# Performance work log

Hardware: AMD Instinct MI355X
Metric: run time of the kernel (lower is better)

Reference implementation:

```python
import jax, jax.numpy as jnp
import numpy as np

DMODEL = 1024
N_EXPERTS = 8
EXPERT_SIZE = 4096
TOPK = 2
B, S = 2, 2048


def setup_inputs() -> dict:
    key = jax.random.key(0)
    ks = jax.random.split(key, 6)
    std = EXPERT_SIZE ** (-0.5)  # init_expert_weights: normal(0, expert_size**-0.5 * weight_scale)
    x = jax.random.normal(ks[0], (B, S, DMODEL), dtype=jnp.float32)
    gate_w = 0.02 * jax.random.normal(ks[1], (N_EXPERTS, DMODEL), dtype=jnp.float32)
    w1 = std * jax.random.normal(ks[2], (N_EXPERTS, EXPERT_SIZE, DMODEL), dtype=jnp.float32)
    b1 = jnp.zeros((N_EXPERTS, EXPERT_SIZE), dtype=jnp.float32)
    w2 = std * jax.random.normal(ks[3], (N_EXPERTS, DMODEL, EXPERT_SIZE), dtype=jnp.float32)
    b2 = jnp.zeros((N_EXPERTS, DMODEL), dtype=jnp.float32)
    return {"x": x, "gate_w": gate_w, "w1": w1, "b1": b1, "w2": w2, "b2": b2}


def reference(x, gate_w, w1, b1, w2, b2):
    # Router: gate linear (no bias) -> softmax -> top-k expert selection
    logits = jnp.einsum('bsd,ed->bse', x, gate_w)          # [B,S,E]
    probs = jax.nn.softmax(logits, axis=-1)                # gate_softmax
    top_w, top_i = jax.lax.top_k(probs, TOPK)              # [B,S,K]
    # Scatter top-k weights back to a dense [B,S,E] routing matrix
    route = jnp.sum(jax.nn.one_hot(top_i, N_EXPERTS, dtype=probs.dtype)
                    * top_w[..., None], axis=-2)           # [B,S,E]
    # Per-expert 2-layer MLP (Linear -> ReLU -> Linear), combined by route weights
    out = jnp.zeros_like(x)
    for e in range(N_EXPERTS):
        h = jax.nn.relu(jnp.einsum('bsd,hd->bsh', x, w1[e]) + b1[e])  # [B,S,H]
        y = jnp.einsum('bsh,dh->bsd', h, w2[e]) + b2[e]               # [B,S,D]
        out = out + route[..., e, None] * y
    return out
```

## Files before the change

kernel.cpp:

```cpp
#include <hip/hip_runtime.h>
#include <hip/hip_bf16.h>
#include <stdint.h>

#define DMODEL 1024
#define NEXP   8
#define HSZ    4096
#define NTOK   4096

typedef __attribute__((ext_vector_type(8))) short bf16x8;
typedef __attribute__((ext_vector_type(4))) float f32x4;

__device__ __forceinline__ unsigned short f2bf(float f) {
  union { float f; unsigned u; } v; v.f = f;
  return (unsigned short)((v.u + 0x8000u) >> 16);
}

__device__ __forceinline__ void gl2lds16(const void* g, void* lds) {
  __builtin_amdgcn_global_load_lds(
      (const __attribute__((address_space(1))) unsigned*)g,
      (__attribute__((address_space(3))) unsigned*)lds, 16, 0, 0);
}

__global__ __launch_bounds__(256) void cvt_all_kernel(
    const float* __restrict__ x, const float* __restrict__ w1,
    const float* __restrict__ w2, unsigned short* __restrict__ xb,
    unsigned short* __restrict__ w1b, unsigned short* __restrict__ w2b) {
  const size_t n0 = (size_t)NTOK * DMODEL / 4;
  const size_t n1 = (size_t)NEXP * HSZ * DMODEL / 4;
  size_t i = (size_t)blockIdx.x * 256 + threadIdx.x;
  const float* src; unsigned short* dst; size_t j;
  if (i < n0)            { src = x;  dst = xb;  j = i; }
  else if (i < n0 + n1)  { src = w1; dst = w1b; j = i - n0; }
  else                   { src = w2; dst = w2b; j = i - n0 - n1; }
  float4 v = ((const float4*)src)[j];
  ((ushort4*)dst)[j] = make_ushort4(f2bf(v.x), f2bf(v.y), f2bf(v.z), f2bf(v.w));
}

__global__ __launch_bounds__(256) void router_kernel(
    const float* __restrict__ x, const float* __restrict__ gw,
    int* __restrict__ cnt, int* __restrict__ tokl, float* __restrict__ twgt,
    int* __restrict__ sidx) {
  int wave = threadIdx.x >> 6;
  int lane = threadIdx.x & 63;
  int t = blockIdx.x * 4 + wave;
  const float* xr = x + (size_t)t * DMODEL;
  float acc[NEXP];
#pragma unroll
  for (int e = 0; e < NEXP; ++e) acc[e] = 0.f;
  for (int d = lane; d < DMODEL; d += 64) {
    float xv = xr[d];
#pragma unroll
    for (int e = 0; e < NEXP; ++e) acc[e] = fmaf(xv, gw[e * DMODEL + d], acc[e]);
  }
#pragma unroll
  for (int e = 0; e < NEXP; ++e) {
#pragma unroll
    for (int o = 32; o > 0; o >>= 1) acc[e] += __shfl_down(acc[e], o);
  }
  if (lane == 0) {
    float m = acc[0];
#pragma unroll
    for (int e = 1; e < NEXP; ++e) m = fmaxf(m, acc[e]);
    float p[NEXP]; float s = 0.f;
#pragma unroll
    for (int e = 0; e < NEXP; ++e) { p[e] = __expf(acc[e] - m); s += p[e]; }
    float inv = 1.f / s;
    int i0 = 0; float b0 = p[0];
#pragma unroll
    for (int e = 1; e < NEXP; ++e) if (p[e] > b0) { b0 = p[e]; i0 = e; }
    int i1 = (i0 == 0) ? 1 : 0; float b1v = p[i1];
#pragma unroll
    for (int e = 0; e < NEXP; ++e) if (e != i0 && p[e] > b1v) { b1v = p[e]; i1 = e; }
    int p0 = atomicAdd(&cnt[i0], 1);
    tokl[i0 * NTOK + p0] = t; twgt[i0 * NTOK + p0] = b0 * inv;
    int p1 = atomicAdd(&cnt[i1], 1);
    tokl[i1 * NTOK + p1] = t; twgt[i1 * NTOK + p1] = b1v * inv;
    sidx[2 * t]     = (i0 << 16) | p0;
    sidx[2 * t + 1] = (i1 << 16) | p1;
  }
}

__global__ __launch_bounds__(256) void gemm1_bf_kernel(
    const unsigned short* __restrict__ Xbf, const unsigned short* __restrict__ W1bf,
    const float* __restrict__ b1, const int* __restrict__ cnt,
    const int* __restrict__ tokl, unsigned short* __restrict__ Hbuf) {
  const int e = blockIdx.z;
  const int ne = cnt[e];
  const int m0 = blockIdx.y * 128;
  if (m0 >= ne) return;
  const int n0 = blockIdx.x * 128;
  int toff = 0;
  for (int i = 0; i < NEXP; ++i) toff += (i < e) ? cnt[i] : 0;

  __shared__ __align__(16) unsigned short As[2][128 * 32];
  __shared__ __align__(16) unsigned short Bs[2][128 * 32];

  const int tid = threadIdx.x;
  const int lane = tid & 63;
  const int wave = tid >> 6;
  const int wm = (wave >> 1) * 64;
  const int wn = (wave & 1) * 64;

  const int srow = wave * 16 + (lane >> 2);
  const int scol = (((lane & 3) ^ ((lane >> 3) & 3)) << 3);
  const int* tlist = tokl + e * NTOK;
  const unsigned short* gA[2]; const unsigned short* gB[2];
  int lofs[2];
#pragma unroll
  for (int c = 0; c < 2; ++c) {
    int r = c * 64 + srow;
    int gr = m0 + r;
    int tk = tlist[(gr < ne) ? gr : 0];
    gA[c] = Xbf + (size_t)tk * DMODEL + scol;
    gB[c] = W1bf + (size_t)e * HSZ * DMODEL + (size_t)(n0 + r) * DMODEL + scol;
    lofs[c] = (c * 64 + wave * 16) * 32;
  }

  f32x4 acc[4][4];
#pragma unroll
  for (int i = 0; i < 4; ++i)
#pragma unroll
    for (int j = 0; j < 4; ++j) acc[i][j] = (f32x4){0.f, 0.f, 0.f, 0.f};

  const int fr = lane & 15;
  const int cb = lane >> 4;

#pragma unroll
  for (int c = 0; c < 2; ++c) {
    gl2lds16(gA[c], &As[0][lofs[c]]);
    gl2lds16(gB[c], &Bs[0][lofs[c]]);
  }
  __syncthreads();

  int cur = 0;
  for (int k0 = 0; k0 < DMODEL; k0 += 32) {
    const int nxt = k0 + 32;
    if (nxt < DMODEL) {
#pragma unroll
      for (int c = 0; c < 2; ++c) {
        gl2lds16(gA[c] + nxt, &As[cur ^ 1][lofs[c]]);
        gl2lds16(gB[c] + nxt, &Bs[cur ^ 1][lofs[c]]);
      }
    }
    bf16x8 af[4], bfg[4];
#pragma unroll
    for (int i = 0; i < 4; ++i) {
      int ar = wm + i * 16 + fr;
      af[i]  = *(const bf16x8*)&As[cur][ar * 32 + ((cb ^ ((ar >> 1) & 3)) << 3)];
      int br = wn + i * 16 + fr;
      bfg[i] = *(const bf16x8*)&Bs[cur][br * 32 + ((cb ^ ((br >> 1) & 3)) << 3)];
    }
#pragma unroll
    for (int i = 0; i < 4; ++i)
#pragma unroll
      for (int j = 0; j < 4; ++j)
        acc[i][j] = __builtin_amdgcn_mfma_f32_16x16x32_bf16(bfg[j], af[i], acc[i][j], 0, 0, 0);
    __syncthreads();
    cur ^= 1;
  }

  const int hq = (lane >> 4) * 4;
#pragma unroll
  for (int i = 0; i < 4; ++i) {
    int trow = m0 + wm + i * 16 + fr;
    if (trow >= ne) continue;
    size_t hrow = (size_t)(toff + trow) * HSZ;
#pragma unroll
    for (int j = 0; j < 4; ++j) {
      int hcol = n0 + wn + j * 16 + hq;
      const float* bp = b1 + e * HSZ + hcol;
      unsigned short u[4];
#pragma unroll
      for (int r = 0; r < 4; ++r)
        u[r] = f2bf(fmaxf(acc[i][j][r] + bp[r], 0.f));
      *(ushort4*)&Hbuf[hrow + hcol] = make_ushort4(u[0], u[1], u[2], u[3]);
    }
  }
}

__global__ __launch_bounds__(256) void gemm2_bf_kernel(
    const unsigned short* __restrict__ Hbuf, const unsigned short* __restrict__ W2bf,
    const float* __restrict__ b2, const int* __restrict__ cnt,
    const float* __restrict__ twgt, float* __restrict__ Ybuf) {
  const int e = blockIdx.z;
  const int ne = cnt[e];
  const int m0 = blockIdx.y * 128;
  if (m0 >= ne) return;
  const int n0 = blockIdx.x * 128;
  int toff = 0;
  for (int i = 0; i < NEXP; ++i) toff += (i < e) ? cnt[i] : 0;

  __shared__ __align__(16) unsigned short As[2][128 * 64];
  __shared__ __align__(16) unsigned short Bs[2][128 * 64];

  const int tid = threadIdx.x;
  const int lane = tid & 63;
  const int wave = tid >> 6;
  const int wm = (wave >> 1) * 64;
  const int wn = (wave & 1) * 64;

  const int srow = (wave << 5) + (lane >> 3);
  const int scb  = (((lane & 7) ^ (lane >> 3)) << 3);
  const unsigned short* gA[4]; const unsigned short* gB[4];
  int lofs[4];
#pragma unroll
  for (int c = 0; c < 4; ++c) {
    int r = srow + c * 8;
    int gr = m0 + r;
    int rc = (gr < ne) ? gr : 0;
    gA[c] = Hbuf + (size_t)(toff + rc) * HSZ + scb;
    gB[c] = W2bf + (size_t)e * DMODEL * HSZ + (size_t)(n0 + r) * HSZ + scb;
    lofs[c] = ((wave << 5) + c * 8) * 64;
  }

  f32x4 acc[4][4];
#pragma unroll
  for (int i = 0; i < 4; ++i)
#pragma unroll
    for (int j = 0; j < 4; ++j) acc[i][j] = (f32x4){0.f, 0.f, 0.f, 0.f};

  const int fr = lane & 15;
  const int cb0 = lane >> 4;

#pragma unroll
  for (int c = 0; c < 4; ++c) {
    gl2lds16(gA[c], &As[0][lofs[c]]);
    gl2lds16(gB[c], &Bs[0][lofs[c]]);
  }
  __syncthreads();

  int cur = 0;
  for (int k0 = 0; k0 < HSZ; k0 += 64) {
    const int nxt = k0 + 64;
    if (nxt < HSZ) {
#pragma unroll
      for (int c = 0; c < 4; ++c) {
        gl2lds16(gA[c] + nxt, &As[cur ^ 1][lofs[c]]);
        gl2lds16(gB[c] + nxt, &Bs[cur ^ 1][lofs[c]]);
      }
    }
    bf16x8 af[2][4], bfg[2][4];
#pragma unroll
    for (int h = 0; h < 2; ++h) {
      int cb = cb0 + h * 4;
#pragma unroll
      for (int i = 0; i < 4; ++i) {
        int ar = wm + i * 16 + fr;
        af[h][i]  = *(const bf16x8*)&As[cur][ar * 64 + ((cb ^ (ar & 7)) << 3)];
        int br = wn + i * 16 + fr;
        bfg[h][i] = *(const bf16x8*)&Bs[cur][br * 64 + ((cb ^ (br & 7)) << 3)];
      }
    }
#pragma unroll
    for (int h = 0; h < 2; ++h)
#pragma unroll
      for (int i = 0; i < 4; ++i)
#pragma unroll
        for (int j = 0; j < 4; ++j)
          acc[i][j] = __builtin_amdgcn_mfma_f32_16x16x32_bf16(bfg[h][j], af[h][i],
                                                              acc[i][j], 0, 0, 0);
    __syncthreads();
    cur ^= 1;
  }

  const float* wlist = twgt + e * NTOK;
  const int dq = (lane >> 4) * 4;
#pragma unroll
  for (int i = 0; i < 4; ++i) {
    int trow = m0 + wm + i * 16 + fr;
    if (trow >= ne) continue;
    float wgt = wlist[trow];
    float* yrow = Ybuf + (size_t)(toff + trow) * DMODEL;
#pragma unroll
    for (int j = 0; j < 4; ++j) {
      int d0 = n0 + wn + j * 16 + dq;
      const float* b2p = b2 + e * DMODEL + d0;
      float4 v = make_float4(wgt * (acc[i][j][0] + b2p[0]),
                             wgt * (acc[i][j][1] + b2p[1]),
                             wgt * (acc[i][j][2] + b2p[2]),
                             wgt * (acc[i][j][3] + b2p[3]));
      *(float4*)(yrow + d0) = v;
    }
  }
}

__global__ __launch_bounds__(256) void combine_kernel(
    const float* __restrict__ Ybuf, const int* __restrict__ cnt,
    const int* __restrict__ sidx, float* __restrict__ out) {
  int t = blockIdx.x;
  int offv[NEXP];
  int s = 0;
#pragma unroll
  for (int e = 0; e < NEXP; ++e) { offv[e] = s; s += cnt[e]; }
  int s0 = sidx[2 * t], s1 = sidx[2 * t + 1];
  size_t r0 = (size_t)(offv[s0 >> 16] + (s0 & 0xffff)) * DMODEL;
  size_t r1 = (size_t)(offv[s1 >> 16] + (s1 & 0xffff)) * DMODEL;
  int c = threadIdx.x * 4;
  float4 a = *(const float4*)(Ybuf + r0 + c);
  float4 b = *(const float4*)(Ybuf + r1 + c);
  *(float4*)(out + (size_t)t * DMODEL + c) =
      make_float4(a.x + b.x, a.y + b.y, a.z + b.z, a.w + b.w);
}

extern "C" void kernel_launch(void* const* d_in, const int* in_sizes, int n_in,
                              void* d_out, int out_size, void* d_ws, size_t ws_size,
                              hipStream_t stream) {
  const float* x  = (const float*)d_in[0];
  const float* gw = (const float*)d_in[1];
  const float* w1 = (const float*)d_in[2];
  const float* b1 = (const float*)d_in[3];
  const float* w2 = (const float*)d_in[4];
  const float* b2 = (const float*)d_in[5];
  float* out = (float*)d_out;

  char* ws = (char*)d_ws;
  int* cnt    = (int*)ws;
  int* tokl   = (int*)(ws + 128);
  float* twgt = (float*)(ws + 128 + NEXP * NTOK * 4);
  int* sidx   = (int*)(ws + 128 + 2 * NEXP * NTOK * 4);

  constexpr size_t OFF_XBF  = 327680;
  constexpr size_t OFF_W1BF = OFF_XBF  + (size_t)NTOK * DMODEL * 2;
  constexpr size_t OFF_W2BF = OFF_W1BF + (size_t)NEXP * HSZ * DMODEL * 2;
  constexpr size_t OFF_HBUF = OFF_W2BF + (size_t)NEXP * DMODEL * HSZ * 2;
  unsigned short* Xbf  = (unsigned short*)(ws + OFF_XBF);
  unsigned short* W1bf = (unsigned short*)(ws + OFF_W1BF);
  unsigned short* W2bf = (unsigned short*)(ws + OFF_W2BF);
  unsigned short* Hbuf = (unsigned short*)(ws + OFF_HBUF);
  float* Ybuf = (float*)(ws + OFF_W1BF);

  hipMemsetAsync(cnt, 0, 32, stream);
  router_kernel<<<NTOK / 4, 256, 0, stream>>>(x, gw, cnt, tokl, twgt, sidx);
  const size_t ncvt = (size_t)NTOK * DMODEL / 4 + 2 * (size_t)NEXP * HSZ * DMODEL / 4;
  cvt_all_kernel<<<(unsigned)((ncvt + 255) / 256), 256, 0, stream>>>(
      x, w1, w2, Xbf, W1bf, W2bf);
  gemm1_bf_kernel<<<dim3(HSZ / 128, NTOK / 128, NEXP), 256, 0, stream>>>(
      Xbf, W1bf, b1, cnt, tokl, Hbuf);
  gemm2_bf_kernel<<<dim3(DMODEL / 128, NTOK / 128, NEXP), 256, 0, stream>>>(
      Hbuf, W2bf, b2, cnt, twgt, Ybuf);
  combine_kernel<<<NTOK, 256, 0, stream>>>(Ybuf, cnt, sidx, out);
}
```

Measured before the change: 673.8 us.

## Split-K the second expert GEMM and batch router atomics per block

```diff
diff --git a/kernel.cpp b/kernel.cpp
--- a/kernel.cpp
+++ b/kernel.cpp
@@ -6,6 +6,7 @@
 #define NEXP   8
 #define HSZ    4096
 #define NTOK   4096
+#define KSPLIT 2
 
 typedef __attribute__((ext_vector_type(8))) short bf16x8;
 typedef __attribute__((ext_vector_type(4))) float f32x4;
@@ -40,43 +41,64 @@
     const float* __restrict__ x, const float* __restrict__ gw,
     int* __restrict__ cnt, int* __restrict__ tokl, float* __restrict__ twgt,
     int* __restrict__ sidx) {
-  int wave = threadIdx.x >> 6;
-  int lane = threadIdx.x & 63;
-  int t = blockIdx.x * 4 + wave;
-  const float* xr = x + (size_t)t * DMODEL;
-  float acc[NEXP];
-#pragma unroll
-  for (int e = 0; e < NEXP; ++e) acc[e] = 0.f;
-  for (int d = lane; d < DMODEL; d += 64) {
-    float xv = xr[d];
-#pragma unroll
-    for (int e = 0; e < NEXP; ++e) acc[e] = fmaf(xv, gw[e * DMODEL + d], acc[e]);
-  }
-#pragma unroll
-  for (int e = 0; e < NEXP; ++e) {
-#pragma unroll
-    for (int o = 32; o > 0; o >>= 1) acc[e] += __shfl_down(acc[e], o);
-  }
-  if (lane == 0) {
-    float m = acc[0];
-#pragma unroll
-    for (int e = 1; e < NEXP; ++e) m = fmaxf(m, acc[e]);
-    float p[NEXP]; float s = 0.f;
-#pragma unroll
-    for (int e = 0; e < NEXP; ++e) { p[e] = __expf(acc[e] - m); s += p[e]; }
-    float inv = 1.f / s;
-    int i0 = 0; float b0 = p[0];
-#pragma unroll
-    for (int e = 1; e < NEXP; ++e) if (p[e] > b0) { b0 = p[e]; i0 = e; }
-    int i1 = (i0 == 0) ? 1 : 0; float b1v = p[i1];
-#pragma unroll
-    for (int e = 0; e < NEXP; ++e) if (e != i0 && p[e] > b1v) { b1v = p[e]; i1 = e; }
-    int p0 = atomicAdd(&cnt[i0], 1);
-    tokl[i0 * NTOK + p0] = t; twgt[i0 * NTOK + p0] = b0 * inv;
-    int p1 = atomicAdd(&cnt[i1], 1);
-    tokl[i1 * NTOK + p1] = t; twgt[i1 * NTOK + p1] = b1v * inv;
-    sidx[2 * t]     = (i0 << 16) | p0;
-    sidx[2 * t + 1] = (i1 << 16) | p1;
+  __shared__ int lcnt[NEXP];
+  __shared__ int lbase[NEXP];
+  __shared__ int rE[64];
+  __shared__ int rS[64];
+  __shared__ float rW[64];
+  const int tid = threadIdx.x;
+  const int wave = tid >> 6;
+  const int lane = tid & 63;
+  if (tid < NEXP) lcnt[tid] = 0;
+  __syncthreads();
+
+  for (int i = 0; i < 8; ++i) {
+    int lt = wave * 8 + i;
+    int t = blockIdx.x * 32 + lt;
+    const float* xr = x + (size_t)t * DMODEL;
+    float acc[NEXP];
+#pragma unroll
+    for (int e = 0; e < NEXP; ++e) acc[e] = 0.f;
+    for (int d = lane; d < DMODEL; d += 64) {
+      float xv = xr[d];
+#pragma unroll
+      for (int e = 0; e < NEXP; ++e) acc[e] = fmaf(xv, gw[e * DMODEL + d], acc[e]);
+    }
+#pragma unroll
+    for (int e = 0; e < NEXP; ++e) {
+#pragma unroll
+      for (int o = 32; o > 0; o >>= 1) acc[e] += __shfl_down(acc[e], o);
+    }
+    if (lane == 0) {
+      float m = acc[0];
+#pragma unroll
+      for (int e = 1; e < NEXP; ++e) m = fmaxf(m, acc[e]);
+      float p[NEXP]; float s = 0.f;
+#pragma unroll
+      for (int e = 0; e < NEXP; ++e) { p[e] = __expf(acc[e] - m); s += p[e]; }
+      float inv = 1.f / s;
+      int i0 = 0; float b0 = p[0];
+#pragma unroll
+      for (int e = 1; e < NEXP; ++e) if (p[e] > b0) { b0 = p[e]; i0 = e; }
+      int i1 = (i0 == 0) ? 1 : 0; float b1v = p[i1];
+#pragma unroll
+      for (int e = 0; e < NEXP; ++e) if (e != i0 && p[e] > b1v) { b1v = p[e]; i1 = e; }
+      int s0l = atomicAdd(&lcnt[i0], 1);
+      rE[lt * 2] = i0; rS[lt * 2] = s0l; rW[lt * 2] = b0 * inv;
+      int s1l = atomicAdd(&lcnt[i1], 1);
+      rE[lt * 2 + 1] = i1; rS[lt * 2 + 1] = s1l; rW[lt * 2 + 1] = b1v * inv;
+    }
+  }
+  __syncthreads();
+  if (tid < NEXP) lbase[tid] = atomicAdd(&cnt[tid], lcnt[tid]);
+  __syncthreads();
+  if (tid < 64) {
+    int e = rE[tid];
+    int p = lbase[e] + rS[tid];
+    int t = blockIdx.x * 32 + (tid >> 1);
+    tokl[e * NTOK + p] = t;
+    twgt[e * NTOK + p] = rW[tid];
+    sidx[2 * t + (tid & 1)] = (e << 16) | p;
   }
 }
 
@@ -180,18 +202,20 @@
 
 __global__ __launch_bounds__(256) void gemm2_bf_kernel(
     const unsigned short* __restrict__ Hbuf, const unsigned short* __restrict__ W2bf,
-    const float* __restrict__ b2, const int* __restrict__ cnt,
-    const float* __restrict__ twgt, float* __restrict__ Ybuf) {
-  const int e = blockIdx.z;
+    const int* __restrict__ cnt, const float* __restrict__ twgt,
+    float* __restrict__ Ybuf) {
+  const int e = blockIdx.z & 7;
+  const int ks = blockIdx.z >> 3;
   const int ne = cnt[e];
   const int m0 = blockIdx.y * 128;
   if (m0 >= ne) return;
   const int n0 = blockIdx.x * 128;
+  const int kbase = ks * (HSZ / KSPLIT);
   int toff = 0;
   for (int i = 0; i < NEXP; ++i) toff += (i < e) ? cnt[i] : 0;
 
-  __shared__ __align__(16) unsigned short As[2][128 * 64];
-  __shared__ __align__(16) unsigned short Bs[2][128 * 64];
+  __shared__ __align__(16) unsigned short As[2][128 * 32];
+  __shared__ __align__(16) unsigned short Bs[2][128 * 32];
 
   const int tid = threadIdx.x;
   const int lane = tid & 63;
@@ -199,18 +223,18 @@
   const int wm = (wave >> 1) * 64;
   const int wn = (wave & 1) * 64;
 
-  const int srow = (wave << 5) + (lane >> 3);
-  const int scb  = (((lane & 7) ^ (lane >> 3)) << 3);
-  const unsigned short* gA[4]; const unsigned short* gB[4];
-  int lofs[4];
-#pragma unroll
-  for (int c = 0; c < 4; ++c) {
-    int r = srow + c * 8;
+  const int srow = wave * 16 + (lane >> 2);
+  const int scol = (((lane & 3) ^ ((lane >> 3) & 3)) << 3);
+  const unsigned short* gA[2]; const unsigned short* gB[2];
+  int lofs[2];
+#pragma unroll
+  for (int c = 0; c < 2; ++c) {
+    int r = c * 64 + srow;
     int gr = m0 + r;
     int rc = (gr < ne) ? gr : 0;
-    gA[c] = Hbuf + (size_t)(toff + rc) * HSZ + scb;
-    gB[c] = W2bf + (size_t)e * DMODEL * HSZ + (size_t)(n0 + r) * HSZ + scb;
-    lofs[c] = ((wave << 5) + c * 8) * 64;
+    gA[c] = Hbuf + (size_t)(toff + rc) * HSZ + kbase + scol;
+    gB[c] = W2bf + (size_t)e * DMODEL * HSZ + (size_t)(n0 + r) * HSZ + kbase + scol;
+    lofs[c] = (c * 64 + wave * 16) * 32;
   }
 
   f32x4 acc[4][4];
@@ -220,86 +244,90 @@
     for (int j = 0; j < 4; ++j) acc[i][j] = (f32x4){0.f, 0.f, 0.f, 0.f};
 
   const int fr = lane & 15;
-  const int cb0 = lane >> 4;
-
-#pragma unroll
-  for (int c = 0; c < 4; ++c) {
+  const int cb = lane >> 4;
+
+#pragma unroll
+  for (int c = 0; c < 2; ++c) {
     gl2lds16(gA[c], &As[0][lofs[c]]);
     gl2lds16(gB[c], &Bs[0][lofs[c]]);
   }
   __syncthreads();
 
   int cur = 0;
-  for (int k0 = 0; k0 < HSZ; k0 += 64) {
-    const int nxt = k0 + 64;
-    if (nxt < HSZ) {
-#pragma unroll
-      for (int c = 0; c < 4; ++c) {
+  for (int k0 = 0; k0 < HSZ / KSPLIT; k0 += 32) {
+    const int nxt = k0 + 32;
+    if (nxt < HSZ / KSPLIT) {
+#pragma unroll
+      for (int c = 0; c < 2; ++c) {
         gl2lds16(gA[c] + nxt, &As[cur ^ 1][lofs[c]]);
         gl2lds16(gB[c] + nxt, &Bs[cur ^ 1][lofs[c]]);
       }
     }
-    bf16x8 af[2][4], bfg[2][4];
-#pragma unroll
-    for (int h = 0; h < 2; ++h) {
-      int cb = cb0 + h * 4;
-#pragma unroll
-      for (int i = 0; i < 4; ++i) {
-        int ar = wm + i * 16 + fr;
-        af[h][i]  = *(const bf16x8*)&As[cur][ar * 64 + ((cb ^ (ar & 7)) << 3)];
-        int br = wn + i * 16 + fr;
-        bfg[h][i] = *(const bf16x8*)&Bs[cur][br * 64 + ((cb ^ (br & 7)) << 3)];
-      }
-    }
-#pragma unroll
-    for (int h = 0; h < 2; ++h)
-#pragma unroll
-      for (int i = 0; i < 4; ++i)
-#pragma unroll
-        for (int j = 0; j < 4; ++j)
-          acc[i][j] = __builtin_amdgcn_mfma_f32_16x16x32_bf16(bfg[h][j], af[h][i],
-                                                              acc[i][j], 0, 0, 0);
+    bf16x8 af[4], bfg[4];
+#pragma unroll
+    for (int i = 0; i < 4; ++i) {
+      int ar = wm + i * 16 + fr;
+      af[i]  = *(const bf16x8*)&As[cur][ar * 32 + ((cb ^ ((ar >> 1) & 3)) << 3)];
+      int br = wn + i * 16 + fr;
+      bfg[i] = *(const bf16x8*)&Bs[cur][br * 32 + ((cb ^ ((br >> 1) & 3)) << 3)];
+    }
+#pragma unroll
+    for (int i = 0; i < 4; ++i)
+#pragma unroll
+      for (int j = 0; j < 4; ++j)
+        acc[i][j] = __builtin_amdgcn_mfma_f32_16x16x32_bf16(bfg[j], af[i], acc[i][j], 0, 0, 0);
     __syncthreads();
     cur ^= 1;
   }
 
   const float* wlist = twgt + e * NTOK;
   const int dq = (lane >> 4) * 4;
+  float* yp = Ybuf + (size_t)ks * (2 * NTOK) * DMODEL;
 #pragma unroll
   for (int i = 0; i < 4; ++i) {
     int trow = m0 + wm + i * 16 + fr;
     if (trow >= ne) continue;
     float wgt = wlist[trow];
-    float* yrow = Ybuf + (size_t)(toff + trow) * DMODEL;
+    float* yrow = yp + (size_t)(toff + trow) * DMODEL;
 #pragma unroll
     for (int j = 0; j < 4; ++j) {
       int d0 = n0 + wn + j * 16 + dq;
-      const float* b2p = b2 + e * DMODEL + d0;
-      float4 v = make_float4(wgt * (acc[i][j][0] + b2p[0]),
-                             wgt * (acc[i][j][1] + b2p[1]),
-                             wgt * (acc[i][j][2] + b2p[2]),
-                             wgt * (acc[i][j][3] + b2p[3]));
+      float4 v = make_float4(wgt * acc[i][j][0], wgt * acc[i][j][1],
+                             wgt * acc[i][j][2], wgt * acc[i][j][3]);
       *(float4*)(yrow + d0) = v;
     }
   }
 }
 
 __global__ __launch_bounds__(256) void combine_kernel(
-    const float* __restrict__ Ybuf, const int* __restrict__ cnt,
-    const int* __restrict__ sidx, float* __restrict__ out) {
+    const float* __restrict__ Ybuf, const float* __restrict__ b2,
+    const int* __restrict__ cnt, const int* __restrict__ sidx,
+    const float* __restrict__ twgt, float* __restrict__ out) {
   int t = blockIdx.x;
   int offv[NEXP];
   int s = 0;
 #pragma unroll
   for (int e = 0; e < NEXP; ++e) { offv[e] = s; s += cnt[e]; }
   int s0 = sidx[2 * t], s1 = sidx[2 * t + 1];
-  size_t r0 = (size_t)(offv[s0 >> 16] + (s0 & 0xffff)) * DMODEL;
-  size_t r1 = (size_t)(offv[s1 >> 16] + (s1 & 0xffff)) * DMODEL;
+  int e0 = s0 >> 16, e1 = s1 >> 16;
+  int sl0 = s0 & 0xffff, sl1 = s1 & 0xffff;
+  size_t r0 = (size_t)(offv[e0] + sl0) * DMODEL;
+  size_t r1 = (size_t)(offv[e1] + sl1) * DMODEL;
+  float w0 = twgt[e0 * NTOK + sl0];
+  float w1 = twgt[e1 * NTOK + sl1];
+  const size_t PSTR = (size_t)(2 * NTOK) * DMODEL;
   int c = threadIdx.x * 4;
-  float4 a = *(const float4*)(Ybuf + r0 + c);
-  float4 b = *(const float4*)(Ybuf + r1 + c);
-  *(float4*)(out + (size_t)t * DMODEL + c) =
-      make_float4(a.x + b.x, a.y + b.y, a.z + b.z, a.w + b.w);
+  float4 a0 = *(const float4*)(Ybuf + r0 + c);
+  float4 a1 = *(const float4*)(Ybuf + PSTR + r0 + c);
+  float4 c0 = *(const float4*)(Ybuf + r1 + c);
+  float4 c1 = *(const float4*)(Ybuf + PSTR + r1 + c);
+  float4 bb0 = *(const float4*)(b2 + (size_t)e0 * DMODEL + c);
+  float4 bb1 = *(const float4*)(b2 + (size_t)e1 * DMODEL + c);
+  *(float4*)(out + (size_t)t * DMODEL + c) = make_float4(
+      a0.x + a1.x + c0.x + c1.x + w0 * bb0.x + w1 * bb1.x,
+      a0.y + a1.y + c0.y + c1.y + w0 * bb0.y + w1 * bb1.y,
+      a0.z + a1.z + c0.z + c1.z + w0 * bb0.z + w1 * bb1.z,
+      a0.w + a1.w + c0.w + c1.w + w0 * bb0.w + w1 * bb1.w);
 }
 
 extern "C" void kernel_launch(void* const* d_in, const int* in_sizes, int n_in,
@@ -330,13 +358,13 @@
   float* Ybuf = (float*)(ws + OFF_W1BF);
 
   hipMemsetAsync(cnt, 0, 32, stream);
-  router_kernel<<<NTOK / 4, 256, 0, stream>>>(x, gw, cnt, tokl, twgt, sidx);
+  router_kernel<<<NTOK / 32, 256, 0, stream>>>(x, gw, cnt, tokl, twgt, sidx);
   const size_t ncvt = (size_t)NTOK * DMODEL / 4 + 2 * (size_t)NEXP * HSZ * DMODEL / 4;
   cvt_all_kernel<<<(unsigned)((ncvt + 255) / 256), 256, 0, stream>>>(
       x, w1, w2, Xbf, W1bf, W2bf);
   gemm1_bf_kernel<<<dim3(HSZ / 128, NTOK / 128, NEXP), 256, 0, stream>>>(
       Xbf, W1bf, b1, cnt, tokl, Hbuf);
-  gemm2_bf_kernel<<<dim3(DMODEL / 128, NTOK / 128, NEXP), 256, 0, stream>>>(
-      Hbuf, W2bf, b2, cnt, twgt, Ybuf);
-  combine_kernel<<<NTOK, 256, 0, stream>>>(Ybuf, cnt, sidx, out);
-}
+  gemm2_bf_kernel<<<dim3(DMODEL / 128, NTOK / 128, NEXP * KSPLIT), 256, 0, stream>>>(
+      Hbuf, W2bf, cnt, twgt, Ybuf);
+  combine_kernel<<<NTOK, 256, 0, stream>>>(Ybuf, b2, cnt, sidx, twgt, out);
+}
```

New measurement: 628.8 us. -6.7%, faster.
